# Kernel optimization log

Hardware: AMD Instinct MI355X
Metric: run time of the kernel (lower is better)

## Reference

```python
import jax, jax.numpy as jnp
import numpy as np

D_MODEL = 1024
N_HEAD = 16
D_K = 64
D_V = 64
SEQ = 4096


def setup_inputs() -> dict:
    key = jax.random.key(0)
    ks = jax.random.split(key, 7)
    s = 1.0 / np.sqrt(D_MODEL)
    return {
        "q": jax.random.normal(ks[0], (SEQ, D_MODEL), dtype=jnp.float32),
        "k": jax.random.normal(ks[1], (SEQ, D_MODEL), dtype=jnp.float32),
        "v": jax.random.normal(ks[2], (SEQ, D_MODEL), dtype=jnp.float32),
        "Wq": jax.random.normal(ks[3], (N_HEAD * D_K, D_MODEL), dtype=jnp.float32) * s,
        "Wk": jax.random.normal(ks[4], (N_HEAD * D_K, D_MODEL), dtype=jnp.float32) * s,
        "Wv": jax.random.normal(ks[5], (N_HEAD * D_V, D_MODEL), dtype=jnp.float32) * s,
        "Wfc": jax.random.normal(ks[6], (D_MODEL, N_HEAD * D_V), dtype=jnp.float32) * s,
    }


def reference(q, k, v, Wq, Wk, Wv, Wfc):
    len_q = q.shape[0]
    residual = q
    temperature = jnp.asarray(np.sqrt(D_K), q.dtype)
    # projections: [len, n_head, d_k] -> [n_head, len, d_k]
    qh = (q @ Wq.T).reshape(len_q, N_HEAD, D_K).transpose(1, 0, 2)
    kh = (k @ Wk.T).reshape(k.shape[0], N_HEAD, D_K).transpose(1, 0, 2)
    vh = (v @ Wv.T).reshape(v.shape[0], N_HEAD, D_V).transpose(1, 0, 2)
    # scores: [n_head, len_q, len_k]
    attn = jnp.einsum('hqd,hkd->hqk', qh / temperature, kh)
    attn = jax.nn.softmax(attn, axis=-1)  # dropout = identity (eval)
    out = jnp.einsum('hqk,hkd->hqd', attn, vh)  # [n_head, len_q, d_v]
    out = out.transpose(1, 0, 2).reshape(len_q, N_HEAD * D_V)
    out = out @ Wfc.T  # dropout = identity (eval)
    return jax.nn.relu(out) + residual
```

## Files before the change

### kernel.cpp

```cpp
#include <hip/hip_runtime.h>
#include <math.h>

#define SEQ    4096
#define DMODEL 1024
#define NHEAD  16
#define DHEAD  64
#define KVHALF 2048

typedef __bf16 bf16;
typedef bf16  bf16x2 __attribute__((ext_vector_type(2)));
typedef bf16  bf16x4 __attribute__((ext_vector_type(4)));
typedef bf16  bf16x8 __attribute__((ext_vector_type(8)));
typedef float f32x4  __attribute__((ext_vector_type(4)));
typedef float f32x16 __attribute__((ext_vector_type(16)));
typedef unsigned int u32;

#define SWZ(r)  ((((r) >> 2) ^ (r)) & 7)
#define SWZ3(r) (((r) ^ ((r) >> 2) ^ ((r) >> 3)) & 7)

__device__ __forceinline__ void gll16(const void* g, void* l) {
    __builtin_amdgcn_global_load_lds(
        (const __attribute__((address_space(1))) void*)g,
        (__attribute__((address_space(3))) void*)l, 16, 0, 0);
}

__device__ __forceinline__ u32 cvtpk(float lo, float hi) {
    u32 r;
    asm("v_cvt_pk_bf16_f32 %0, %1, %2" : "=v"(r) : "v"(lo), "v"(hi));
    return r;
}
__device__ __forceinline__ void pswap(u32& a, u32& b) {
    asm volatile("v_permlane32_swap_b32 %0, %1" : "+v"(a), "+v"(b));
}

__global__ __launch_bounds__(256)
void cvt_bf16(const float* __restrict__ s, bf16* __restrict__ d, int n)
{
    const int i = (blockIdx.x * 256 + threadIdx.x) * 8;
    if (i >= n) return;
    float4 a = *(const float4*)&s[i];
    float4 b = *(const float4*)&s[i + 4];
    bf16x8 v;
    v[0] = (bf16)a.x; v[1] = (bf16)a.y; v[2] = (bf16)a.z; v[3] = (bf16)a.w;
    v[4] = (bf16)b.x; v[5] = (bf16)b.y; v[6] = (bf16)b.z; v[7] = (bf16)b.w;
    *(bf16x8*)&d[i] = v;
}

template<int EPI>
__global__ __launch_bounds__(256)
void gemm_mfma(const bf16* __restrict__ A, const bf16* __restrict__ B,
               bf16* __restrict__ Cb, float* __restrict__ Cf,
               const float* __restrict__ res, int M, int N, int K)
{
    const int bm   = blockIdx.y * 64;
    const int bn   = blockIdx.x * 64;
    const int tid  = threadIdx.x;
    const int w    = tid >> 6;
    const int lane = tid & 63;
    const int lr   = lane & 15;
    const int lh   = lane >> 4;
    const int wr   = w >> 1;
    const int wc   = w & 1;
    const int lrow = lane >> 3;
    const int lch  = lane & 7;

    __shared__ bf16 As[64 * 64];
    __shared__ bf16 Bs[64 * 64];

    f32x4 acc[2][2] = {};

    for (int k0 = 0; k0 < K; k0 += 64) {
        __syncthreads();
        #pragma unroll
        for (int i = 0; i < 2; ++i) {
            const int r = (w * 2 + i) * 8 + lrow;
            gll16(A + (size_t)(bm + r) * K + k0 + ((lch ^ SWZ(r)) << 3),
                  &As[(w * 2 + i) * 512]);
        }
        #pragma unroll
        for (int i = 0; i < 2; ++i) {
            const int r = (w * 2 + i) * 8 + lrow;
            gll16(B + (size_t)(bn + r) * K + k0 + ((lch ^ SWZ(r)) << 3),
                  &Bs[(w * 2 + i) * 512]);
        }
        asm volatile("s_waitcnt vmcnt(0)" ::: "memory");
        __syncthreads();

        bf16x8 af[2][2], bfr[2][2];
        #pragma unroll
        for (int rt = 0; rt < 2; ++rt)
            #pragma unroll
            for (int s = 0; s < 2; ++s) {
                const int r = wr * 32 + rt * 16 + lr;
                af[rt][s] = *(const bf16x8*)&As[r * 64 + (((s * 4 + lh) ^ SWZ(r)) << 3)];
            }
        #pragma unroll
        for (int ct = 0; ct < 2; ++ct)
            #pragma unroll
            for (int s = 0; s < 2; ++s) {
                const int r = wc * 32 + ct * 16 + lr;
                bfr[ct][s] = *(const bf16x8*)&Bs[r * 64 + (((s * 4 + lh) ^ SWZ(r)) << 3)];
            }
        __builtin_amdgcn_s_setprio(1);
        #pragma unroll
        for (int rt = 0; rt < 2; ++rt)
            #pragma unroll
            for (int ct = 0; ct < 2; ++ct)
                #pragma unroll
                for (int s = 0; s < 2; ++s)
                    acc[rt][ct] = __builtin_amdgcn_mfma_f32_16x16x32_bf16(
                        af[rt][s], bfr[ct][s], acc[rt][ct], 0, 0, 0);
        __builtin_amdgcn_s_setprio(0);
    }

    #pragma unroll
    for (int rt = 0; rt < 2; ++rt)
        #pragma unroll
        for (int ct = 0; ct < 2; ++ct)
            #pragma unroll
            for (int r = 0; r < 4; ++r) {
                const int m = bm + wr * 32 + rt * 16 + lh * 4 + r;
                const int n = bn + wc * 32 + ct * 16 + lr;
                if (EPI == 0) {
                    Cb[(size_t)m * N + n] = (bf16)acc[rt][ct][r];
                } else {
                    Cf[(size_t)m * N + n] =
                        fmaxf(acc[rt][ct][r], 0.f) + res[(size_t)m * N + n];
                }
            }
}

__global__ __launch_bounds__(256, 4)
void attn_mfma(const bf16* __restrict__ Q, const bf16* __restrict__ K,
               const bf16* __restrict__ V,
               bf16* __restrict__ Oa, bf16* __restrict__ Ob,
               float* __restrict__ La, float* __restrict__ Lb)
{
    const int wg   = blockIdx.x;
    const int lgc  = (wg & 7) * 128 + (wg >> 3);
    const int half = lgc >> 9;
    const int h    = (lgc >> 5) & 15;
    const int q0   = (lgc & 31) * 128;
    const int c0   = half * KVHALF;

    bf16*  Op = half ? Ob : Oa;
    float* Lp = half ? Lb : La;

    const int tid  = threadIdx.x;
    const int w    = tid >> 6;
    const int lane = tid & 63;
    const int lo5  = lane & 31;
    const int hi   = lane >> 5;
    const int lrow = lane >> 3;
    const int lch  = lane & 7;

    __shared__ bf16 Ks[2][64 * 64];
    __shared__ bf16 Vt[2][64 * 64];

    const bf16* qrow = Q + (size_t)(q0 + w * 32 + lo5) * DMODEL + h * 64;
    bf16x8 qf[4];
    #pragma unroll
    for (int s = 0; s < 4; ++s)
        qf[s] = *(const bf16x8*)&qrow[s * 16 + hi * 8];

    f32x16 acc0 = {}, acc1 = {};
    float lsum = 0.f;

    const int vk = (tid & 7) * 8;
    const int vd = (tid >> 3) * 2;

    const float SC = 0.18033688f;

    #pragma unroll
    for (int i = 0; i < 2; ++i) {
        const int r = (w * 2 + i) * 8 + lrow;
        gll16(K + (size_t)(c0 + r) * DMODEL + h * 64 + ((lch ^ SWZ3(r)) << 3),
              &Ks[0][(w * 2 + i) * 512]);
    }
    {
        bf16x2 u[8];
        #pragma unroll
        for (int i = 0; i < 8; ++i)
            u[i] = *(const bf16x2*)&V[(size_t)(c0 + vk + i) * DMODEL + h * 64 + vd];
        asm volatile("s_waitcnt vmcnt(0)" ::: "memory");
        bf16x8 v0, v1;
        #pragma unroll
        for (int i = 0; i < 8; ++i) { v0[i] = u[i][0]; v1[i] = u[i][1]; }
        *(bf16x8*)&Vt[0][(vd + 0) * 64 + (((tid & 7) ^ SWZ3(vd + 0)) << 3)] = v0;
        *(bf16x8*)&Vt[0][(vd + 1) * 64 + (((tid & 7) ^ SWZ3(vd + 1)) << 3)] = v1;
    }
    __syncthreads();

#define BODY(CUR, CN)                                                          \
    {                                                                          \
        const int cn = c0 + (((CN) - c0) & (KVHALF - 1));                      \
        _Pragma("unroll")                                                      \
        for (int i = 0; i < 2; ++i) {                                          \
            const int r = (w * 2 + i) * 8 + lrow;                              \
            gll16(K + (size_t)(cn + r) * DMODEL + h * 64 + ((lch ^ SWZ3(r)) << 3), \
                  &Ks[(CUR) ^ 1][(w * 2 + i) * 512]);                          \
        }                                                                      \
        bf16x2 u[8];                                                           \
        _Pragma("unroll")                                                      \
        for (int i = 0; i < 8; ++i)                                            \
            u[i] = *(const bf16x2*)&V[(size_t)(cn + vk + i) * DMODEL + h * 64 + vd]; \
        const bf16* Kc = Ks[CUR];                                              \
        const bf16* Vc = Vt[CUR];                                              \
        _Pragma("unroll")                                                      \
        for (int kh = 0; kh < 2; ++kh) {                                       \
            const int rr = kh * 32 + lo5;                                      \
            f32x16 st = {};                                                    \
            __builtin_amdgcn_s_setprio(1);                                     \
            _Pragma("unroll")                                                  \
            for (int s = 0; s < 4; ++s) {                                      \
                bf16x8 kf = *(const bf16x8*)&Kc[rr * 64 + (((s * 2 + hi) ^ SWZ3(rr)) << 3)]; \
                st = __builtin_amdgcn_mfma_f32_32x32x16_bf16(kf, qf[s], st, 0, 0, 0); \
            }                                                                  \
            __builtin_amdgcn_s_setprio(0);                                     \
            _Pragma("unroll")                                                  \
            for (int r = 0; r < 16; ++r)                                       \
                st[r] = __builtin_amdgcn_exp2f(fminf(st[r] * SC, 50.f));       \
            lsum += (((st[0] + st[1]) + (st[2] + st[3]))                       \
                   + ((st[4] + st[5]) + (st[6] + st[7])))                      \
                  + (((st[8] + st[9]) + (st[10] + st[11]))                     \
                   + ((st[12] + st[13]) + (st[14] + st[15])));                 \
            _Pragma("unroll")                                                  \
            for (int kk = 0; kk < 2; ++kk) {                                   \
                const int ks = kh * 2 + kk;                                    \
                const int b = kk * 8;                                          \
                u32 A0 = cvtpk(st[b + 0], st[b + 1]);                          \
                u32 C0 = cvtpk(st[b + 2], st[b + 3]);                          \
                u32 B0 = cvtpk(st[b + 4], st[b + 5]);                          \
                u32 D0 = cvtpk(st[b + 6], st[b + 7]);                          \
                pswap(A0, B0);                                                 \
                pswap(C0, D0);                                                 \
                union { u32 wd[4]; bf16x8 v; } fr;                             \
                fr.wd[0] = A0; fr.wd[1] = C0; fr.wd[2] = B0; fr.wd[3] = D0;    \
                bf16x8 vf0 = *(const bf16x8*)&Vc[lo5 * 64 + (((ks * 2 + hi) ^ SWZ3(lo5)) << 3)]; \
                bf16x8 vf1 = *(const bf16x8*)&Vc[(32 + lo5) * 64 + (((ks * 2 + hi) ^ SWZ3(32 + lo5)) << 3)]; \
                __builtin_amdgcn_s_setprio(1);                                 \
                acc0 = __builtin_amdgcn_mfma_f32_32x32x16_bf16(vf0, fr.v, acc0, 0, 0, 0); \
                acc1 = __builtin_amdgcn_mfma_f32_32x32x16_bf16(vf1, fr.v, acc1, 0, 0, 0); \
                __builtin_amdgcn_s_setprio(0);                                 \
            }                                                                  \
        }                                                                      \
        asm volatile("s_waitcnt vmcnt(0)" ::: "memory");                       \
        {                                                                      \
            bf16x8 v0, v1;                                                     \
            _Pragma("unroll")                                                  \
            for (int i = 0; i < 8; ++i) { v0[i] = u[i][0]; v1[i] = u[i][1]; }  \
            bf16* Vn = Vt[(CUR) ^ 1];                                          \
            *(bf16x8*)&Vn[(vd + 0) * 64 + (((tid & 7) ^ SWZ3(vd + 0)) << 3)] = v0; \
            *(bf16x8*)&Vn[(vd + 1) * 64 + (((tid & 7) ^ SWZ3(vd + 1)) << 3)] = v1; \
        }                                                                      \
        __syncthreads();                                                       \
    }

    for (int c = c0; c < c0 + KVHALF; c += 128) {
        BODY(0, c + 64)
        BODY(1, c + 128)
    }
#undef BODY

    float lt = lsum;
    lt += __shfl_xor(lt, 32);
    Lp[h * SEQ + q0 + w * 32 + lo5] = lt;

    bf16* orow = Op + (size_t)(q0 + w * 32 + lo5) * DMODEL + h * 64;
    #pragma unroll
    for (int g = 0; g < 4; ++g) {
        bf16x4 o4;
        o4[0] = (bf16)acc0[g * 4 + 0];
        o4[1] = (bf16)acc0[g * 4 + 1];
        o4[2] = (bf16)acc0[g * 4 + 2];
        o4[3] = (bf16)acc0[g * 4 + 3];
        *(bf16x4*)&orow[g * 8 + 4 * hi] = o4;
        bf16x4 o5;
        o5[0] = (bf16)acc1[g * 4 + 0];
        o5[1] = (bf16)acc1[g * 4 + 1];
        o5[2] = (bf16)acc1[g * 4 + 2];
        o5[3] = (bf16)acc1[g * 4 + 3];
        *(bf16x4*)&orow[32 + g * 8 + 4 * hi] = o5;
    }
}

__global__ __launch_bounds__(256)
void combine(const bf16* __restrict__ Oa, const bf16* __restrict__ Ob,
             const float* __restrict__ La, const float* __restrict__ Lb,
             bf16* __restrict__ AO)
{
    const int e   = (blockIdx.x * 256 + threadIdx.x) * 8;
    const int row = e >> 10;
    const int hh  = (e >> 6) & 15;
    const float inv = 1.0f / (La[hh * SEQ + row] + Lb[hh * SEQ + row]);
    bf16x8 a = *(const bf16x8*)&Oa[e];
    bf16x8 b = *(const bf16x8*)&Ob[e];
    bf16x8 o;
    #pragma unroll
    for (int i = 0; i < 8; ++i)
        o[i] = (bf16)(((float)a[i] + (float)b[i]) * inv);
    *(bf16x8*)&AO[e] = o;
}

extern "C" void kernel_launch(void* const* d_in, const int* in_sizes, int n_in,
                              void* d_out, int out_size, void* d_ws, size_t ws_size,
                              hipStream_t stream)
{
    const float* q   = (const float*)d_in[0];
    const float* k   = (const float*)d_in[1];
    const float* v   = (const float*)d_in[2];
    const float* Wq  = (const float*)d_in[3];
    const float* Wk  = (const float*)d_in[4];
    const float* Wv  = (const float*)d_in[5];
    const float* Wfc = (const float*)d_in[6];
    float* out = (float*)d_out;

    const int EM = SEQ * DMODEL;
    const int WM = DMODEL * DMODEL;

    bf16* Wfcb = (bf16*)d_ws;
    bf16* qb   = Wfcb + WM;
    bf16* kb   = qb + EM;
    bf16* vb   = kb + EM;
    bf16* Wqb  = vb + EM;
    bf16* Wkb  = Wqb + WM;
    bf16* Wvb  = Wkb + WM;
    bf16* Pq   = Wvb + WM;
    bf16* Pk   = Pq + EM;
    bf16* Pv   = Pk + EM;
    bf16* AO   = Pv + EM;

    bf16*  Oa = qb;
    bf16*  Ob = kb;
    float* La = (float*)vb;
    float* Lb = La + NHEAD * SEQ;

    cvt_bf16<<<EM / 2048, 256, 0, stream>>>(q,   qb,   EM);
    cvt_bf16<<<EM / 2048, 256, 0, stream>>>(k,   kb,   EM);
    cvt_bf16<<<EM / 2048, 256, 0, stream>>>(v,   vb,   EM);
    cvt_bf16<<<WM / 2048, 256, 0, stream>>>(Wq,  Wqb,  WM);
    cvt_bf16<<<WM / 2048, 256, 0, stream>>>(Wk,  Wkb,  WM);
    cvt_bf16<<<WM / 2048, 256, 0, stream>>>(Wv,  Wvb,  WM);
    cvt_bf16<<<WM / 2048, 256, 0, stream>>>(Wfc, Wfcb, WM);

    dim3 gg(DMODEL / 64, SEQ / 64);
    gemm_mfma<0><<<gg, 256, 0, stream>>>(qb, Wqb, Pq, nullptr, nullptr, SEQ, DMODEL, DMODEL);
    gemm_mfma<0><<<gg, 256, 0, stream>>>(kb, Wkb, Pk, nullptr, nullptr, SEQ, DMODEL, DMODEL);
    gemm_mfma<0><<<gg, 256, 0, stream>>>(vb, Wvb, Pv, nullptr, nullptr, SEQ, DMODEL, DMODEL);

    attn_mfma<<<1024, 256, 0, stream>>>(Pq, Pk, Pv, Oa, Ob, La, Lb);

    combine<<<EM / 2048, 256, 0, stream>>>(Oa, Ob, La, Lb, AO);

    gemm_mfma<1><<<gg, 256, 0, stream>>>(AO, Wfcb, nullptr, out, q, SEQ, DMODEL, DMODEL);
}
```

Measured before the change: 214.0 us.

## Produce transposed V projection in GEMM and async-load V tiles into LDS

The V projection GEMM now computes Wv·vᵀ directly, so V is stored transposed (head-dim by sequence) in global memory. The attention kernel then loads V tiles straight into LDS with global_load_lds, replacing register-staged bf16x2 loads and the in-register transpose plus LDS writes. Both 32-key score tiles are computed up front so their MFMAs can interleave. This removes per-iteration VALU and LDS-store overhead and strided small V loads, at the cost of higher register pressure from the two live score tiles.

New measurement: 240.5 us. 1.12x slower.

```diff
diff --git a/kernel.cpp b/kernel.cpp
--- a/kernel.cpp
+++ b/kernel.cpp
@@ -132,7 +132,7 @@
 
 __global__ __launch_bounds__(256, 4)
 void attn_mfma(const bf16* __restrict__ Q, const bf16* __restrict__ K,
-               const bf16* __restrict__ V,
+               const bf16* __restrict__ Vt_g,
                bf16* __restrict__ Oa, bf16* __restrict__ Ob,
                float* __restrict__ La, float* __restrict__ Lb)
 {
@@ -166,9 +166,6 @@
     f32x16 acc0 = {}, acc1 = {};
     float lsum = 0.f;
 
-    const int vk = (tid & 7) * 8;
-    const int vd = (tid >> 3) * 2;
-
     const float SC = 0.18033688f;
 
     #pragma unroll
@@ -176,62 +173,70 @@
         const int r = (w * 2 + i) * 8 + lrow;
         gll16(K + (size_t)(c0 + r) * DMODEL + h * 64 + ((lch ^ SWZ3(r)) << 3),
               &Ks[0][(w * 2 + i) * 512]);
-    }
-    {
-        bf16x2 u[8];
-        #pragma unroll
-        for (int i = 0; i < 8; ++i)
-            u[i] = *(const bf16x2*)&V[(size_t)(c0 + vk + i) * DMODEL + h * 64 + vd];
-        asm volatile("s_waitcnt vmcnt(0)" ::: "memory");
-        bf16x8 v0, v1;
-        #pragma unroll
-        for (int i = 0; i < 8; ++i) { v0[i] = u[i][0]; v1[i] = u[i][1]; }
-        *(bf16x8*)&Vt[0][(vd + 0) * 64 + (((tid & 7) ^ SWZ3(vd + 0)) << 3)] = v0;
-        *(bf16x8*)&Vt[0][(vd + 1) * 64 + (((tid & 7) ^ SWZ3(vd + 1)) << 3)] = v1;
-    }
+        gll16(Vt_g + (size_t)(h * 64 + r) * SEQ + c0 + ((lch ^ SWZ3(r)) << 3),
+              &Vt[0][(w * 2 + i) * 512]);
+    }
+    asm volatile("s_waitcnt vmcnt(0)" ::: "memory");
     __syncthreads();
 
 #define BODY(CUR, CN)                                                          \
     {                                                                          \
         const int cn = c0 + (((CN) - c0) & (KVHALF - 1));                      \
+                         \
         _Pragma("unroll")                                                      \
         for (int i = 0; i < 2; ++i) {                                          \
             const int r = (w * 2 + i) * 8 + lrow;                              \
             gll16(K + (size_t)(cn + r) * DMODEL + h * 64 + ((lch ^ SWZ3(r)) << 3), \
                   &Ks[(CUR) ^ 1][(w * 2 + i) * 512]);                          \
+            gll16(Vt_g + (size_t)(h * 64 + r) * SEQ + cn + ((lch ^ SWZ3(r)) << 3), \
+                  &Vt[(CUR) ^ 1][(w * 2 + i) * 512]);                          \
         }                                                                      \
-        bf16x2 u[8];                                                           \
-        _Pragma("unroll")                                                      \
-        for (int i = 0; i < 8; ++i)                                            \
-            u[i] = *(const bf16x2*)&V[(size_t)(cn + vk + i) * DMODEL + h * 64 + vd]; \
         const bf16* Kc = Ks[CUR];                                              \
         const bf16* Vc = Vt[CUR];                                              \
+                          \
+        f32x16 st0 = {}, st1 = {};                                             \
+        __builtin_amdgcn_s_setprio(1);                                         \
+        _Pragma("unroll")                                                      \
+        for (int s = 0; s < 4; ++s) {                                          \
+            bf16x8 kf0 = *(const bf16x8*)&Kc[lo5 * 64 + (((s * 2 + hi) ^ SWZ3(lo5)) << 3)]; \
+            bf16x8 kf1 = *(const bf16x8*)&Kc[(32 + lo5) * 64 + (((s * 2 + hi) ^ SWZ3(32 + lo5)) << 3)]; \
+            st0 = __builtin_amdgcn_mfma_f32_32x32x16_bf16(kf0, qf[s], st0, 0, 0, 0); \
+            st1 = __builtin_amdgcn_mfma_f32_32x32x16_bf16(kf1, qf[s], st1, 0, 0, 0); \
+        }                                                                      \
+        __builtin_amdgcn_s_setprio(0);                                         \
+                                              \
+        _Pragma("unroll")                                                      \
+        for (int r = 0; r < 16; ++r) {                                         \
+            st0[r] = __builtin_amdgcn_exp2f(fminf(st0[r] * SC, 50.f));         \
+            st1[r] = __builtin_amdgcn_exp2f(fminf(st1[r] * SC, 50.f));         \
+        }                                                                      \
+        lsum += (((st0[0] + st0[1]) + (st0[2] + st0[3]))                       \
+               + ((st0[4] + st0[5]) + (st0[6] + st0[7])))                      \
+              + (((st0[8] + st0[9]) + (st0[10] + st0[11]))                     \
+               + ((st0[12] + st0[13]) + (st0[14] + st0[15])));                 \
+        lsum += (((st1[0] + st1[1]) + (st1[2] + st1[3]))                       \
+               + ((st1[4] + st1[5]) + (st1[6] + st1[7])))                      \
+              + (((st1[8] + st1[9]) + (st1[10] + st1[11]))                     \
+               + ((st1[12] + st1[13]) + (st1[14] + st1[15])));                 \
+                   \
         _Pragma("unroll")                                                      \
         for (int kh = 0; kh < 2; ++kh) {                                       \
-            const int rr = kh * 32 + lo5;                                      \
-            f32x16 st = {};                                                    \
-            __builtin_amdgcn_s_setprio(1);                                     \
-            _Pragma("unroll")                                                  \
-            for (int s = 0; s < 4; ++s) {                                      \
-                bf16x8 kf = *(const bf16x8*)&Kc[rr * 64 + (((s * 2 + hi) ^ SWZ3(rr)) << 3)]; \
-                st = __builtin_amdgcn_mfma_f32_32x32x16_bf16(kf, qf[s], st, 0, 0, 0); \
-            }                                                                  \
-            __builtin_amdgcn_s_setprio(0);                                     \
-            _Pragma("unroll")                                                  \
-            for (int r = 0; r < 16; ++r)                                       \
-                st[r] = __builtin_amdgcn_exp2f(fminf(st[r] * SC, 50.f));       \
-            lsum += (((st[0] + st[1]) + (st[2] + st[3]))                       \
-                   + ((st[4] + st[5]) + (st[6] + st[7])))                      \
-                  + (((st[8] + st[9]) + (st[10] + st[11]))                     \
-                   + ((st[12] + st[13]) + (st[14] + st[15])));                 \
             _Pragma("unroll")                                                  \
             for (int kk = 0; kk < 2; ++kk) {                                   \
                 const int ks = kh * 2 + kk;                                    \
                 const int b = kk * 8;                                          \
-                u32 A0 = cvtpk(st[b + 0], st[b + 1]);                          \
-                u32 C0 = cvtpk(st[b + 2], st[b + 3]);                          \
-                u32 B0 = cvtpk(st[b + 4], st[b + 5]);                          \
-                u32 D0 = cvtpk(st[b + 6], st[b + 7]);                          \
+                u32 A0, B0, C0, D0;                                            \
+                if (kh == 0) {                                                 \
+                    A0 = cvtpk(st0[b + 0], st0[b + 1]);                        \
+                    C0 = cvtpk(st0[b + 2], st0[b + 3]);                        \
+                    B0 = cvtpk(st0[b + 4], st0[b + 5]);                        \
+                    D0 = cvtpk(st0[b + 6], st0[b + 7]);                        \
+                } else {                                                       \
+                    A0 = cvtpk(st1[b + 0], st1[b + 1]);                        \
+                    C0 = cvtpk(st1[b + 2], st1[b + 3]);                        \
+                    B0 = cvtpk(st1[b + 4], st1[b + 5]);                        \
+                    D0 = cvtpk(st1[b + 6], st1[b + 7]);                        \
+                }                                                              \
                 pswap(A0, B0);                                                 \
                 pswap(C0, D0);                                                 \
                 union { u32 wd[4]; bf16x8 v; } fr;                             \
@@ -245,14 +250,6 @@
             }                                                                  \
         }                                                                      \
         asm volatile("s_waitcnt vmcnt(0)" ::: "memory");                       \
-        {                                                                      \
-            bf16x8 v0, v1;                                                     \
-            _Pragma("unroll")                                                  \
-            for (int i = 0; i < 8; ++i) { v0[i] = u[i][0]; v1[i] = u[i][1]; }  \
-            bf16* Vn = Vt[(CUR) ^ 1];                                          \
-            *(bf16x8*)&Vn[(vd + 0) * 64 + (((tid & 7) ^ SWZ3(vd + 0)) << 3)] = v0; \
-            *(bf16x8*)&Vn[(vd + 1) * 64 + (((tid & 7) ^ SWZ3(vd + 1)) << 3)] = v1; \
-        }                                                                      \
         __syncthreads();                                                       \
     }
 
@@ -327,8 +324,8 @@
     bf16* Wvb  = Wkb + WM;
     bf16* Pq   = Wvb + WM;
     bf16* Pk   = Pq + EM;
-    bf16* Pv   = Pk + EM;
-    bf16* AO   = Pv + EM;
+    bf16* Pvt  = Pk + EM;
+    bf16* AO   = Pvt + EM;
 
     bf16*  Oa = qb;
     bf16*  Ob = kb;
@@ -346,9 +343,10 @@
     dim3 gg(DMODEL / 64, SEQ / 64);
     gemm_mfma<0><<<gg, 256, 0, stream>>>(qb, Wqb, Pq, nullptr, nullptr, SEQ, DMODEL, DMODEL);
     gemm_mfma<0><<<gg, 256, 0, stream>>>(kb, Wkb, Pk, nullptr, nullptr, SEQ, DMODEL, DMODEL);
-    gemm_mfma<0><<<gg, 256, 0, stream>>>(vb, Wvb, Pv, nullptr, nullptr, SEQ, DMODEL, DMODEL);
-
-    attn_mfma<<<1024, 256, 0, stream>>>(Pq, Pk, Pv, Oa, Ob, La, Lb);
+    dim3 ggv(SEQ / 64, DMODEL / 64);
+    gemm_mfma<0><<<ggv, 256, 0, stream>>>(Wvb, vb, Pvt, nullptr, nullptr, DMODEL, SEQ, DMODEL);
+
+    attn_mfma<<<1024, 256, 0, stream>>>(Pq, Pk, Pvt, Oa, Ob, La, Lb);
 
     combine<<<EM / 2048, 256, 0, stream>>>(Oa, Ob, La, Lb, AO);
 
```
